# Kernel tuning notes

Measured on AMD Instinct MI355X. Metric: run time of the kernel, lower is better.

## Reference

```python
import jax, jax.numpy as jnp
import numpy as np

EMBED = 768
HEADS = 12
HEAD_DIM = EMBED // HEADS
FFN = 4 * EMBED
EPS = 1e-5


def setup_inputs() -> dict:
    key = jax.random.key(0)
    ks = jax.random.split(key, 12)
    s = 0.02
    inp = {
        'x': jax.random.normal(ks[0], (1, 4096, EMBED), dtype=jnp.float32),
        'Wq': jax.random.normal(ks[1], (EMBED, EMBED), dtype=jnp.float32) * s,
        'bq': jnp.zeros((EMBED,), jnp.float32),
        'Wk': jax.random.normal(ks[2], (EMBED, EMBED), dtype=jnp.float32) * s,
        'bk': jnp.zeros((EMBED,), jnp.float32),
        'Wv': jax.random.normal(ks[3], (EMBED, EMBED), dtype=jnp.float32) * s,
        'bv': jnp.zeros((EMBED,), jnp.float32),
        'Wo': jax.random.normal(ks[4], (EMBED, EMBED), dtype=jnp.float32) * s,
        'bo': jnp.zeros((EMBED,), jnp.float32),
        'ln1_g': jnp.ones((EMBED,), jnp.float32),
        'ln1_b': jnp.zeros((EMBED,), jnp.float32),
        'W1': jax.random.normal(ks[5], (EMBED, FFN), dtype=jnp.float32) * s,
        'b1': jnp.zeros((FFN,), jnp.float32),
        'W2': jax.random.normal(ks[6], (FFN, EMBED), dtype=jnp.float32) * s,
        'b2': jnp.zeros((EMBED,), jnp.float32),
        'ln2_g': jnp.ones((EMBED,), jnp.float32),
        'ln2_b': jnp.zeros((EMBED,), jnp.float32),
    }
    return inp


def _layernorm(x, g, b):
    mu = jnp.mean(x, axis=-1, keepdims=True)
    var = jnp.mean(jnp.square(x - mu), axis=-1, keepdims=True)
    return (x - mu) * jax.lax.rsqrt(var + EPS) * g + b


def reference(x, Wq, bq, Wk, bk, Wv, bv, Wo, bo, ln1_g, ln1_b, W1, b1, W2, b2, ln2_g, ln2_b):
    B, S, D = x.shape
    # QKV projections -> [B, H, S, d]
    def split_heads(t):
        return t.reshape(B, S, HEADS, HEAD_DIM).transpose(0, 2, 1, 3)
    q = split_heads(x @ Wq + bq)
    k = split_heads(x @ Wk + bk)
    v = split_heads(x @ Wv + bv)
    scores = jnp.einsum('bhqd,bhkd->bhqk', q, k) / np.sqrt(HEAD_DIM).astype(np.float32)
    attn = jax.nn.softmax(scores, axis=-1)
    ctx = jnp.einsum('bhqk,bhkd->bhqd', attn, v)
    ctx = ctx.transpose(0, 2, 1, 3).reshape(B, S, D)
    attn_out = ctx @ Wo + bo
    h = _layernorm(x + attn_out, ln1_g, ln1_b)
    ffn = jax.nn.gelu(h @ W1 + b1, approximate=False) @ W2 + b2
    return _layernorm(h + ffn, ln2_g, ln2_b)
```

## Files before the change

kernel.cpp:

```cpp
#include <hip/hip_runtime.h>
#include <hip/hip_bf16.h>

typedef __attribute__((ext_vector_type(8))) short s16x8;
typedef __attribute__((ext_vector_type(4))) int   i32x4;
typedef __attribute__((ext_vector_type(4))) float f32x4;
typedef __attribute__((ext_vector_type(8))) __bf16 bf16x8;
typedef __attribute__((ext_vector_type(4))) __bf16 bf16x4;

__device__ __forceinline__ short f2bf(float f) {
  unsigned u = __builtin_bit_cast(unsigned, f);
  u = (u + 0x7FFFu + ((u >> 16) & 1u)) >> 16;
  return (short)u;
}
__device__ __forceinline__ float bf2f(short s) {
  unsigned u = ((unsigned)(unsigned short)s) << 16;
  return __builtin_bit_cast(float, u);
}
__device__ __forceinline__ f32x4 mfma16(s16x8 a, s16x8 b, f32x4 c) {
  return __builtin_amdgcn_mfma_f32_16x16x32_bf16(
      __builtin_bit_cast(bf16x8, a), __builtin_bit_cast(bf16x8, b), c, 0, 0, 0);
}
__device__ __forceinline__ void gload16(const void* g, void* l) {
  __builtin_amdgcn_global_load_lds(
      (const __attribute__((address_space(1))) void*)g,
      (__attribute__((address_space(3))) void*)l, 16, 0, 0);
}

__global__ __launch_bounds__(256) void convert_x_kernel(const float* __restrict__ src,
                                                        short* __restrict__ dst, int n8) {
  int i = blockIdx.x * 256 + threadIdx.x;
  if (i >= n8) return;
  float4 v0 = ((const float4*)src)[i * 2];
  float4 v1 = ((const float4*)src)[i * 2 + 1];
  s16x8 o;
  o[0] = f2bf(v0.x); o[1] = f2bf(v0.y); o[2] = f2bf(v0.z); o[3] = f2bf(v0.w);
  o[4] = f2bf(v1.x); o[5] = f2bf(v1.y); o[6] = f2bf(v1.z); o[7] = f2bf(v1.w);
  *(s16x8*)&dst[i * 8] = o;
}

__global__ __launch_bounds__(256) void bconcat_kernel(const float* __restrict__ bq,
                                                      const float* __restrict__ bk,
                                                      const float* __restrict__ bv,
                                                      float* __restrict__ out) {
  int i = blockIdx.x * 256 + threadIdx.x;
  if (i < 2304) out[i] = i < 768 ? bq[i] : (i < 1536 ? bk[i - 768] : bv[i - 1536]);
}

__global__ __launch_bounds__(256) void wconv_kernel(const float* __restrict__ src,
                                                    short* __restrict__ dst, int K, int N) {
  __shared__ float t[32][33];
  int n0 = blockIdx.x * 32, k0 = blockIdx.y * 32;
  int tx = threadIdx.x & 31, ty = threadIdx.x >> 5;
#pragma unroll
  for (int r = 0; r < 4; ++r) t[ty + r * 8][tx] = src[(long)(k0 + ty + r * 8) * N + n0 + tx];
  __syncthreads();
#pragma unroll
  for (int r = 0; r < 4; ++r)
    dst[(long)(n0 + ty + r * 8) * K + k0 + tx] = f2bf(t[tx][ty + r * 8]);
}

__global__ __launch_bounds__(256) void vtrans_kernel(const short* __restrict__ qkv,
                                                     short* __restrict__ vt) {
  __shared__ short t[32][34];
  int c0 = blockIdx.x * 32, s0 = blockIdx.y * 32;
  int tx = threadIdx.x & 31, ty = threadIdx.x >> 5;
#pragma unroll
  for (int r = 0; r < 4; ++r)
    t[ty + r * 8][tx] = qkv[(long)(s0 + ty + r * 8) * 2304 + 1536 + c0 + tx];
  __syncthreads();
#pragma unroll
  for (int r = 0; r < 4; ++r)
    vt[(long)(c0 + ty + r * 8) * 4096 + s0 + tx] = t[tx][ty + r * 8];
}

template <int OUT_MODE>
__global__ __launch_bounds__(256) void gemm_kernel(const short* __restrict__ A,
                                                   const short* __restrict__ Bt,
                                                   const float* __restrict__ bias,
                                                   void* __restrict__ Cout,
                                                   int M, int N, int Kfull, int Ksub) {
  __shared__ short As[2][128 * 32];
  __shared__ short Bs[2][128 * 32];
  const int tid = threadIdx.x;
  const int wave = tid >> 6, lane = tid & 63;
  const int lr = lane & 15, lg = lane >> 4;
  const int wm = wave >> 1, wn = wave & 1;
  const int bm = blockIdx.x, bn = blockIdx.y;
  const long koff = (long)blockIdx.z * Ksub;

  f32x4 acc[4][4] = {};

  const int r0 = tid >> 2;
  const int cc = (tid & 3) * 8;
  const short* Ag0 = A + (long)(bm * 128 + r0) * Kfull + koff + cc;
  const short* Ag1 = Ag0 + (long)64 * Kfull;
  const short* Bg0 = Bt + (long)(bn * 128 + r0) * Kfull + koff + cc;
  const short* Bg1 = Bg0 + (long)64 * Kfull;

  auto STAGE = [&](int buf, int k0) {
    gload16(Ag0 + k0, &As[buf][tid * 8]);
    gload16(Ag1 + k0, &As[buf][64 * 32 + tid * 8]);
    gload16(Bg0 + k0, &Bs[buf][tid * 8]);
    gload16(Bg1 + k0, &Bs[buf][64 * 32 + tid * 8]);
  };
  auto COMPUTE = [&](int buf) {
    s16x8 af[4], bfr[4];
#pragma unroll
    for (int m = 0; m < 4; ++m) {
      int row = wm * 64 + m * 16 + lr;
      af[m] = *(const s16x8*)&As[buf][row * 32 + lg * 8];
    }
#pragma unroll
    for (int n = 0; n < 4; ++n) {
      int row = wn * 64 + n * 16 + lr;
      bfr[n] = *(const s16x8*)&Bs[buf][row * 32 + lg * 8];
    }
#pragma unroll
    for (int m = 0; m < 4; ++m)
#pragma unroll
      for (int n = 0; n < 4; ++n)
        acc[m][n] = mfma16(af[m], bfr[n], acc[m][n]);
  };

  const int nt = Ksub >> 5;
  STAGE(0, 0);
  int cur = 0;
  for (int t = 0; t < nt - 1; ++t) {
    STAGE(cur ^ 1, (t + 1) * 32);
    asm volatile("s_waitcnt vmcnt(4)" ::: "memory");
    __builtin_amdgcn_s_barrier();
    __builtin_amdgcn_sched_barrier(0);
    COMPUTE(cur);
    __builtin_amdgcn_s_barrier();
    cur ^= 1;
  }
  asm volatile("s_waitcnt vmcnt(0)" ::: "memory");
  __builtin_amdgcn_s_barrier();
  __builtin_amdgcn_sched_barrier(0);
  COMPUTE(cur);

  const int gr0 = bm * 128 + wm * 64 + lg * 4;
  const int gc0 = bn * 128 + wn * 64 + lr;
  float* outF = (float*)Cout + (long)blockIdx.z * M * N;
#pragma unroll
  for (int n = 0; n < 4; ++n) {
    int col = gc0 + n * 16;
    float bb = (blockIdx.z == 0) ? bias[col] : 0.f;
#pragma unroll
    for (int m = 0; m < 4; ++m) {
#pragma unroll
      for (int j = 0; j < 4; ++j) {
        int row = gr0 + m * 16 + j;
        float v = acc[m][n][j] + bb;
        if (OUT_MODE == 2) v = 0.5f * v * (1.0f + erff(v * 0.70710678118f));
        if (OUT_MODE == 1) outF[(long)row * N + col] = v;
        else ((short*)Cout)[(long)row * N + col] = f2bf(v);
      }
    }
  }
}

__global__ __launch_bounds__(256) void flash_kernel(const short* __restrict__ qkv,
                                                    const short* __restrict__ vt,
                                                    float* __restrict__ Opart,
                                                    float* __restrict__ Lpart) {
  __shared__ short Kt[2][64 * 64];
  __shared__ short Vs[2][64 * 64];
  __shared__ short Ps[128 * 72];
  const int tid = threadIdx.x;
  const int wave = tid >> 6, lane = tid & 63;
  const int lr = lane & 15, lg = lane >> 4;
  const int lb = blockIdx.x + 32 * blockIdx.y + 384 * blockIdx.z;
  const int nlb = (lb & 7) * 96 + (lb >> 3);
  const int qb = nlb & 31;
  const int h = (nlb >> 5) % 12;
  const int sp = nlb / 384;
  const int qc = h * 64;
  const int hc = 768 + h * 64;
  const int vr = h * 64;
  const float QSCALE = 0.125f * 1.44269504088896f;

  i32x4 kr[2], vrg[2];
  auto LOADREGS = [&](int s0) {
#pragma unroll
    for (int i = 0; i < 2; ++i) {
      int c = tid + i * 256, row = c >> 3, ch = c & 7;
      kr[i] = *(const i32x4*)&qkv[(long)(s0 + row) * 2304 + hc + ch * 8];
      vrg[i] = *(const i32x4*)&vt[(long)(vr + row) * 4096 + s0 + ch * 8];
    }
  };
  auto WRITELDS = [&](int buf) {
#pragma unroll
    for (int i = 0; i < 2; ++i) {
      int c = tid + i * 256, row = c >> 3, ch = c & 7;
      int sc = ch ^ (row & 7);
      *(i32x4*)&Kt[buf][row * 64 + sc * 8] = kr[i];
      *(i32x4*)&Vs[buf][row * 64 + sc * 8] = vrg[i];
    }
  };

  const int sbase = sp * 2048;
  LOADREGS(sbase);

#pragma unroll
  for (int i = 0; i < 4; ++i) {
    int c = tid + i * 256;
    int row = c >> 3, cq = (c & 7) * 8;
    *(i32x4*)&Ps[row * 72 + cq] =
        *(const i32x4*)&qkv[(long)(qb * 128 + row) * 2304 + qc + cq];
  }
  asm volatile("s_waitcnt vmcnt(0)" ::: "memory");
  WRITELDS(0);
  LOADREGS(sbase + 64);
  asm volatile("s_waitcnt lgkmcnt(0)" ::: "memory");
  __builtin_amdgcn_s_barrier();
  __builtin_amdgcn_sched_barrier(0);

  s16x8 qf[2][2];
#pragma unroll
  for (int m = 0; m < 2; ++m)
#pragma unroll
    for (int ks = 0; ks < 2; ++ks) {
      int row = wave * 32 + m * 16 + lr;
      s16x8 v = *(const s16x8*)&Ps[row * 72 + ks * 32 + lg * 8];
#pragma unroll
      for (int e = 0; e < 8; ++e) {
        __bf16 b = (__bf16)(bf2f(v[e]) * QSCALE);
        v[e] = (short)__builtin_bit_cast(unsigned short, b);
      }
      qf[m][ks] = v;
    }

  float l_part[2] = {0.f, 0.f};
  f32x4 oacc[2][4] = {};

  int cur = 0;
  for (int it = 0; it < 32; ++it) {
    f32x4 sacc[2][4] = {};
#pragma unroll
    for (int ks = 0; ks < 2; ++ks) {
      s16x8 kf[4];
#pragma unroll
      for (int n = 0; n < 4; ++n) {
        int row = n * 16 + lr;
        int chk = (ks * 4 + lg) ^ (lr & 7);
        kf[n] = *(const s16x8*)&Kt[cur][row * 64 + chk * 8];
      }
      __builtin_amdgcn_s_setprio(1);
#pragma unroll
      for (int m = 0; m < 2; ++m)
#pragma unroll
        for (int n = 0; n < 4; ++n)
          sacc[m][n] = mfma16(kf[n], qf[m][ks], sacc[m][n]);
      __builtin_amdgcn_s_setprio(0);
    }
#pragma unroll
    for (int m = 0; m < 2; ++m) {
      const int prow = wave * 32 + m * 16 + lr;
      float rs = 0.f;
#pragma unroll
      for (int n = 0; n < 4; ++n) {
        float p0 = __builtin_amdgcn_exp2f(sacc[m][n][0]);
        float p1 = __builtin_amdgcn_exp2f(sacc[m][n][1]);
        float p2 = __builtin_amdgcn_exp2f(sacc[m][n][2]);
        float p3 = __builtin_amdgcn_exp2f(sacc[m][n][3]);
        rs += (p0 + p1) + (p2 + p3);
        bf16x4 pk;
        pk[0] = (__bf16)p0; pk[1] = (__bf16)p1;
        pk[2] = (__bf16)p2; pk[3] = (__bf16)p3;
        *(bf16x4*)&Ps[prow * 72 + n * 16 + lg * 4] = pk;
      }
      l_part[m] += rs;
    }
#pragma unroll
    for (int ks = 0; ks < 2; ++ks) {
      s16x8 pf[2], vf[4];
#pragma unroll
      for (int m = 0; m < 2; ++m) {
        int row = wave * 32 + m * 16 + lr;
        pf[m] = *(const s16x8*)&Ps[row * 72 + ks * 32 + lg * 8];
      }
#pragma unroll
      for (int n = 0; n < 4; ++n) {
        int row = n * 16 + lr;
        int chk = (ks * 4 + lg) ^ (lr & 7);
        vf[n] = *(const s16x8*)&Vs[cur][row * 64 + chk * 8];
      }
      __builtin_amdgcn_s_setprio(1);
#pragma unroll
      for (int m = 0; m < 2; ++m)
#pragma unroll
        for (int n = 0; n < 4; ++n)
          oacc[m][n] = mfma16(pf[m], vf[n], oacc[m][n]);
      __builtin_amdgcn_s_setprio(0);
    }
    if (it < 31) {
      asm volatile("s_waitcnt vmcnt(0)" ::: "memory");
      WRITELDS(cur ^ 1);
      if (it < 30) LOADREGS(sbase + (it + 2) * 64);
      asm volatile("s_waitcnt lgkmcnt(0)" ::: "memory");
      __builtin_amdgcn_s_barrier();
      __builtin_amdgcn_sched_barrier(0);
      cur ^= 1;
    }
  }

  const long pbase = ((long)(h * 32 + qb) * 2 + sp) * 128;
#pragma unroll
  for (int m = 0; m < 2; ++m) {
    float l = l_part[m];
    l += __shfl_xor(l, 16);
    l += __shfl_xor(l, 32);
    if (lane < 16) Lpart[pbase + wave * 32 + m * 16 + lr] = l;
  }
#pragma unroll
  for (int m = 0; m < 2; ++m)
#pragma unroll
    for (int n = 0; n < 4; ++n)
#pragma unroll
      for (int j = 0; j < 4; ++j) {
        int row = wave * 32 + m * 16 + lg * 4 + j;
        Opart[(pbase + row) * 64 + n * 16 + lr] = oacc[m][n][j];
      }
}

__global__ __launch_bounds__(256) void combine_kernel(const float* __restrict__ Opart,
                                                      const float* __restrict__ Lpart,
                                                      short* __restrict__ ctx) {
  const int row = blockIdx.x;
  const int col = blockIdx.y * 256 + threadIdx.x;
  const int h = col >> 6, c = col & 63;
  const int qb = row >> 7, r = row & 127;
  const long p0 = ((long)(h * 32 + qb) * 2) * 128 + r;
  const long p1 = p0 + 128;
  float l = Lpart[p0] + Lpart[p1];
  float o = Opart[p0 * 64 + c] + Opart[p1 * 64 + c];
  ctx[(long)row * 768 + col] = f2bf(o / l);
}

__global__ __launch_bounds__(256) void ln_kernel(const float* __restrict__ a,
                                                 const float* __restrict__ b,
                                                 const float* __restrict__ c,
                                                 const float* __restrict__ g,
                                                 const float* __restrict__ be,
                                                 float* __restrict__ of,
                                                 short* __restrict__ ob) {
  const int row = blockIdx.x;
  const int tid = threadIdx.x;
  const long base = (long)row * 768;
  float v[3];
  float s1 = 0.f, s2 = 0.f;
#pragma unroll
  for (int kk = 0; kk < 3; ++kk) {
    int i = tid + kk * 256;
    float x = a[base + i] + b[base + i] + c[base + i];
    v[kk] = x;
    s1 += x;
    s2 += x * x;
  }
#pragma unroll
  for (int off = 1; off < 64; off <<= 1) {
    s1 += __shfl_xor(s1, off);
    s2 += __shfl_xor(s2, off);
  }
  __shared__ float ws1[4], ws2[4];
  int wave = tid >> 6;
  if ((tid & 63) == 0) { ws1[wave] = s1; ws2[wave] = s2; }
  __syncthreads();
  s1 = ws1[0] + ws1[1] + ws1[2] + ws1[3];
  s2 = ws2[0] + ws2[1] + ws2[2] + ws2[3];
  float mean = s1 * (1.f / 768.f);
  float var = s2 * (1.f / 768.f) - mean * mean;
  float rstd = rsqrtf(var + 1e-5f);
#pragma unroll
  for (int kk = 0; kk < 3; ++kk) {
    int i = tid + kk * 256;
    float o = (v[kk] - mean) * rstd * g[i] + be[i];
    if (of) of[base + i] = o;
    if (ob) ob[base + i] = f2bf(o);
  }
}

extern "C" void kernel_launch(void* const* d_in, const int* in_sizes, int n_in,
                              void* d_out, int out_size, void* d_ws, size_t ws_size,
                              hipStream_t stream) {
  const float* x   = (const float*)d_in[0];
  const float* Wq  = (const float*)d_in[1];
  const float* bq  = (const float*)d_in[2];
  const float* Wk  = (const float*)d_in[3];
  const float* bk  = (const float*)d_in[4];
  const float* Wv  = (const float*)d_in[5];
  const float* bv  = (const float*)d_in[6];
  const float* Wo  = (const float*)d_in[7];
  const float* bo  = (const float*)d_in[8];
  const float* g1  = (const float*)d_in[9];
  const float* be1 = (const float*)d_in[10];
  const float* W1  = (const float*)d_in[11];
  const float* b1  = (const float*)d_in[12];
  const float* W2  = (const float*)d_in[13];
  const float* b2  = (const float*)d_in[14];
  const float* g2  = (const float*)d_in[15];
  const float* be2 = (const float*)d_in[16];

  char* ws = (char*)d_ws;
  size_t off = 0;
  auto alloc = [&](size_t bytes) {
    char* p = ws + off;
    off += (bytes + 255) & ~(size_t)255;
    return p;
  };
  short* xb     = (short*)alloc(4096ul * 768 * 2);
  short* wqkv_t = (short*)alloc(2304ul * 768 * 2);
  short* wo_t   = (short*)alloc(768ul * 768 * 2);
  short* w1_t   = (short*)alloc(3072ul * 768 * 2);
  short* w2_t   = (short*)alloc(768ul * 3072 * 2);
  float* bqkv   = (float*)alloc(2304ul * 4);
  short* qkv    = (short*)alloc(4096ul * 2304 * 2);
  short* vt     = (short*)alloc(768ul * 4096 * 2);
  short* ctx    = (short*)alloc(4096ul * 768 * 2);
  float* attn_o = (float*)alloc(4096ul * 768 * 4);
  short* h_b    = (short*)alloc(4096ul * 768 * 2);
  float* h_f    = (float*)alloc(4096ul * 768 * 4);
  short* f1     = (short*)alloc(4096ul * 3072 * 2);
  float* Opart  = (float*)f1;
  float* Lpart  = (float*)attn_o;
  float* attn_p = (float*)qkv;
  float* ffn_p  = (float*)qkv;

  convert_x_kernel<<<1536, 256, 0, stream>>>(x, xb, 4096 * 768 / 8);
  bconcat_kernel<<<9, 256, 0, stream>>>(bq, bk, bv, bqkv);
  wconv_kernel<<<dim3(24, 24), 256, 0, stream>>>(Wq, wqkv_t, 768, 768);
  wconv_kernel<<<dim3(24, 24), 256, 0, stream>>>(Wk, wqkv_t + 768 * 768, 768, 768);
  wconv_kernel<<<dim3(24, 24), 256, 0, stream>>>(Wv, wqkv_t + 2 * 768 * 768, 768, 768);
  wconv_kernel<<<dim3(24, 24), 256, 0, stream>>>(Wo, wo_t, 768, 768);
  wconv_kernel<<<dim3(96, 24), 256, 0, stream>>>(W1, w1_t, 768, 3072);
  wconv_kernel<<<dim3(24, 96), 256, 0, stream>>>(W2, w2_t, 3072, 768);

  gemm_kernel<0><<<dim3(32, 18), 256, 0, stream>>>(xb, wqkv_t, bqkv, qkv, 4096, 2304, 768, 768);
  vtrans_kernel<<<dim3(24, 128), 256, 0, stream>>>(qkv, vt);
  flash_kernel<<<dim3(32, 12, 2), 256, 0, stream>>>(qkv, vt, Opart, Lpart);
  combine_kernel<<<dim3(4096, 3), 256, 0, stream>>>(Opart, Lpart, ctx);
  gemm_kernel<1><<<dim3(32, 6, 2), 256, 0, stream>>>(ctx, wo_t, bo, attn_p, 4096, 768, 768, 384);
  ln_kernel<<<4096, 256, 0, stream>>>(x, attn_p, attn_p + 4096ul * 768, g1, be1, h_f, h_b);
  gemm_kernel<2><<<dim3(32, 24), 256, 0, stream>>>(h_b, w1_t, b1, f1, 4096, 3072, 768, 768);
  gemm_kernel<1><<<dim3(32, 6, 2), 256, 0, stream>>>(f1, w2_t, b2, ffn_p, 4096, 768, 3072, 1536);
  ln_kernel<<<4096, 256, 0, stream>>>(h_f, ffn_p, ffn_p + 4096ul * 768, g2, be2, (float*)d_out, nullptr);
}
```

Measured before the change: 241.3 us.

## Swizzle GEMM LDS tiles to avoid bank conflicts and move attention prefetch earlier

The GEMM shared-memory tiles change from a 128x32 row layout to a 64x64 layout with an XOR swizzle on 16-byte chunks. Staging addresses and fragment reads are remapped to match, which is meant to cut LDS bank conflicts on the fragment reads. In the attention kernel, the wait for global loads, the write of the next K/V tile to LDS and the issue of the following prefetch now happen before the PV MFMA loop instead of after it. That lets the LDS writes and global loads overlap with the matrix math. The risk is correctness if the swizzle mapping is wrong, plus the early vmcnt(0) wait stalling before the MFMAs.

```diff
diff --git a/kernel.cpp b/kernel.cpp
--- a/kernel.cpp
+++ b/kernel.cpp
@@ -79,8 +79,8 @@
                                                    const float* __restrict__ bias,
                                                    void* __restrict__ Cout,
                                                    int M, int N, int Kfull, int Ksub) {
-  __shared__ short As[2][128 * 32];
-  __shared__ short Bs[2][128 * 32];
+  __shared__ short As[2][64 * 64];
+  __shared__ short Bs[2][64 * 64];
   const int tid = threadIdx.x;
   const int wave = tid >> 6, lane = tid & 63;
   const int lr = lane & 15, lg = lane >> 4;
@@ -90,30 +90,40 @@
 
   f32x4 acc[4][4] = {};
 
-  const int r0 = tid >> 2;
-  const int cc = (tid & 3) * 8;
-  const short* Ag0 = A + (long)(bm * 128 + r0) * Kfull + koff + cc;
-  const short* Ag1 = Ag0 + (long)64 * Kfull;
-  const short* Bg0 = Bt + (long)(bn * 128 + r0) * Kfull + koff + cc;
-  const short* Bg1 = Bg0 + (long)64 * Kfull;
+  const short* Ab = A + (long)bm * 128 * Kfull + koff;
+  const short* Bb = Bt + (long)bn * 128 * Kfull + koff;
+
+  int sj[2], sr[2], skc[2];
+#pragma unroll
+  for (int rnd = 0; rnd < 2; ++rnd) {
+    int c = tid + rnd * 256;
+    int j = c >> 3, c7 = c & 7;
+    int u = c7 ^ (j & 7);
+    sj[rnd] = c;
+    sr[rnd] = j + ((u >> 2) << 6);
+    skc[rnd] = (u & 3) * 8;
+  }
 
   auto STAGE = [&](int buf, int k0) {
-    gload16(Ag0 + k0, &As[buf][tid * 8]);
-    gload16(Ag1 + k0, &As[buf][64 * 32 + tid * 8]);
-    gload16(Bg0 + k0, &Bs[buf][tid * 8]);
-    gload16(Bg1 + k0, &Bs[buf][64 * 32 + tid * 8]);
+#pragma unroll
+    for (int rnd = 0; rnd < 2; ++rnd) {
+      gload16(Ab + (long)sr[rnd] * Kfull + k0 + skc[rnd], &As[buf][sj[rnd] * 8]);
+      gload16(Bb + (long)sr[rnd] * Kfull + k0 + skc[rnd], &Bs[buf][sj[rnd] * 8]);
+    }
   };
   auto COMPUTE = [&](int buf) {
     s16x8 af[4], bfr[4];
 #pragma unroll
     for (int m = 0; m < 4; ++m) {
-      int row = wm * 64 + m * 16 + lr;
-      af[m] = *(const s16x8*)&As[buf][row * 32 + lg * 8];
+      int j = m * 16 + lr;
+      int c7 = ((wm << 2) | lg) ^ (lr & 7);
+      af[m] = *(const s16x8*)&As[buf][j * 64 + c7 * 8];
     }
 #pragma unroll
     for (int n = 0; n < 4; ++n) {
-      int row = wn * 64 + n * 16 + lr;
-      bfr[n] = *(const s16x8*)&Bs[buf][row * 32 + lg * 8];
+      int j = n * 16 + lr;
+      int c7 = ((wn << 2) | lg) ^ (lr & 7);
+      bfr[n] = *(const s16x8*)&Bs[buf][j * 64 + c7 * 8];
     }
 #pragma unroll
     for (int m = 0; m < 4; ++m)
@@ -272,6 +282,12 @@
       }
       l_part[m] += rs;
     }
+    if (it < 31) {
+      asm volatile("s_waitcnt vmcnt(0)" ::: "memory");
+      WRITELDS(cur ^ 1);
+      if (it < 30) LOADREGS(sbase + (it + 2) * 64);
+      __builtin_amdgcn_sched_barrier(0);
+    }
 #pragma unroll
     for (int ks = 0; ks < 2; ++ks) {
       s16x8 pf[2], vf[4];
@@ -295,9 +311,6 @@
       __builtin_amdgcn_s_setprio(0);
     }
     if (it < 31) {
-      asm volatile("s_waitcnt vmcnt(0)" ::: "memory");
-      WRITELDS(cur ^ 1);
-      if (it < 30) LOADREGS(sbase + (it + 2) * 64);
       asm volatile("s_waitcnt lgkmcnt(0)" ::: "memory");
       __builtin_amdgcn_s_barrier();
       __builtin_amdgcn_sched_barrier(0);
```

After: 241.2 us. No clear change (-0.1%).
